# Optimization experiments

Measured on AMD Instinct MI355X. Metric: run time of the kernel, lower is better.

## Reference

```python
import math
import jax, jax.numpy as jnp
import numpy as np

NA = 50000   # number of query nodes
NB = 50000   # number of key/value nodes
E = 800000   # number of edges
CA = 256
CB = 256
D = 256
H = 8
DH = D // H


def setup_inputs() -> dict:
    key = jax.random.key(0)
    ks = jax.random.split(key, 8)
    s = 1.0 / math.sqrt(CA)
    return {
        "Fa": jax.random.normal(ks[0], (NA, CA), dtype=jnp.float32),
        "Fb": jax.random.normal(ks[1], (NB, CB), dtype=jnp.float32),
        "a_idx": jax.random.randint(ks[2], (E,), 0, NA, dtype=jnp.int64)
        if jax.config.jax_enable_x64 else jax.random.randint(ks[2], (E,), 0, NA, dtype=jnp.int32),
        "b_idx": jax.random.randint(ks[3], (E,), 0, NB, dtype=jnp.int64)
        if jax.config.jax_enable_x64 else jax.random.randint(ks[3], (E,), 0, NB, dtype=jnp.int32),
        # torch nn.Linear weights: (out_features, in_features), y = x @ W.T
        "Wq": jax.random.normal(ks[4], (D, CA), dtype=jnp.float32) * s,
        "Wk": jax.random.normal(ks[5], (D, CB), dtype=jnp.float32) * s,
        "Wv": jax.random.normal(ks[6], (D, CB), dtype=jnp.float32) * s,
        "Wproj": jax.random.normal(ks[7], (CA, D), dtype=jnp.float32) * s,
    }


def _edge_attention(Q, K, V, Q_idx, K_idx, n_queries):
    # Q: (Na,H,dh)  K,V: (Nb,H,dh)  Q_idx,K_idx: (E,)
    scale = 1.0 / math.sqrt(Q.shape[-1])
    logits = jnp.sum(Q[Q_idx] * K[K_idx], axis=-1) * scale      # (E, H)
    # segmented softmax over edges sharing the same query (per head)
    seg_max = jax.ops.segment_max(logits, Q_idx, num_segments=n_queries)  # (Na, H)
    seg_max = jnp.where(jnp.isfinite(seg_max), seg_max, 0.0)
    ex = jnp.exp(logits - seg_max[Q_idx])                        # (E, H)
    seg_sum = jax.ops.segment_sum(ex, Q_idx, num_segments=n_queries)      # (Na, H)
    weights = ex / jnp.maximum(seg_sum[Q_idx], 1e-30)            # (E, H)
    # scatter-add weighted values
    out = jax.ops.segment_sum(weights[..., None] * V[K_idx], Q_idx,
                              num_segments=n_queries)            # (Na, H, dh)
    return out


def reference(Fa, Fb, a_idx, b_idx, Wq, Wk, Wv, Wproj):
    Na = Fa.shape[0]
    Q = (Fa @ Wq.T).reshape(Na, H, DH)
    K = (Fb @ Wk.T).reshape(-1, H, DH)
    V = (Fb @ Wv.T).reshape(-1, H, DH)
    out = _edge_attention(Q, K, V, a_idx, b_idx, Na)
    out = out.reshape(Na, H * DH)
    return Fa + out @ Wproj.T
```

## Files before the change

kernel.cpp:

```cpp
#include <hip/hip_runtime.h>

#define DM 256

typedef __attribute__((ext_vector_type(8))) short bf16x8;
typedef __attribute__((ext_vector_type(4))) float f32x4;
typedef __attribute__((ext_vector_type(4))) unsigned short us16x4;
typedef unsigned short us16;

__device__ __forceinline__ unsigned short f2bf(float f) {
  unsigned int u = __float_as_uint(f);
  u += 0x7fffu + ((u >> 16) & 1u);
  return (unsigned short)(u >> 16);
}
__device__ __forceinline__ float bf2f(unsigned short s) {
  return __uint_as_float(((unsigned int)s) << 16);
}

__device__ __forceinline__ void gload16(const void* g, void* l) {
  __builtin_amdgcn_global_load_lds(
      (const __attribute__((address_space(1))) void*)g,
      (__attribute__((address_space(3))) void*)l, 16, 0, 0);
}

template <bool A_FP32>
__global__ __launch_bounds__(512) void gemm_bf16(
    const void* __restrict__ Avoid, const us16* __restrict__ W,
    us16* __restrict__ Cb, float* __restrict__ Cf, const float* __restrict__ R,
    int Mreal, int ldc)
{
  __shared__ us16 As[128 * 32];
  __shared__ us16 Bs[256 * 32];
  const int tid = threadIdx.x;
  const int w = tid >> 6, l = tid & 63;
  const int wr = w >> 2, wc = w & 3;
  const int rowBase = blockIdx.x * 128;
  const int colBase = blockIdx.y * 256;
  const int ar = tid >> 2, ac = (tid & 3) * 8;
  f32x4 acc[4][4] = {};

  for (int k0 = 0; k0 < 256; k0 += 32) {
#pragma unroll
    for (int j = 0; j < 2; ++j) {
      const int r0 = (w * 2 + j) * 16;
      gload16(W + (size_t)(colBase + r0 + (l >> 2)) * 256 + k0 + (l & 3) * 8,
              &Bs[r0 * 32]);
    }
    {
      const int grow = rowBase + ar;
      bf16x8 av = (bf16x8){0, 0, 0, 0, 0, 0, 0, 0};
      if (grow < Mreal) {
        if (A_FP32) {
          const float* Af = (const float*)Avoid;
          const float4 x = *(const float4*)(Af + (size_t)grow * 256 + k0 + ac);
          const float4 y = *(const float4*)(Af + (size_t)grow * 256 + k0 + ac + 4);
          av[0] = (short)f2bf(x.x); av[1] = (short)f2bf(x.y);
          av[2] = (short)f2bf(x.z); av[3] = (short)f2bf(x.w);
          av[4] = (short)f2bf(y.x); av[5] = (short)f2bf(y.y);
          av[6] = (short)f2bf(y.z); av[7] = (short)f2bf(y.w);
        } else {
          const us16* Ab = (const us16*)Avoid;
          av = *(const bf16x8*)(Ab + (size_t)grow * 256 + k0 + ac);
        }
      }
      *(bf16x8*)&As[ar * 32 + ac] = av;
    }
    __syncthreads();
    bf16x8 af[4], bfr[4];
#pragma unroll
    for (int m = 0; m < 4; ++m)
      af[m] = *(const bf16x8*)&As[(wr * 64 + m * 16 + (l & 15)) * 32 + (l >> 4) * 8];
#pragma unroll
    for (int n = 0; n < 4; ++n)
      bfr[n] = *(const bf16x8*)&Bs[(wc * 64 + n * 16 + (l & 15)) * 32 + (l >> 4) * 8];
#pragma unroll
    for (int m = 0; m < 4; ++m)
#pragma unroll
      for (int n = 0; n < 4; ++n)
        acc[m][n] = __builtin_amdgcn_mfma_f32_16x16x32_bf16(af[m], bfr[n], acc[m][n], 0, 0, 0);
    __syncthreads();
  }

  const int er = (l >> 4) * 4;
  const int ec = l & 15;
#pragma unroll
  for (int m = 0; m < 4; ++m)
#pragma unroll
    for (int n = 0; n < 4; ++n)
#pragma unroll
      for (int j = 0; j < 4; ++j) {
        const int grow = rowBase + wr * 64 + m * 16 + er + j;
        const int gcol = colBase + wc * 64 + n * 16 + ec;
        const float v = acc[m][n][j];
        if (Cf) {
          if (grow < Mreal) {
            const size_t off = (size_t)grow * ldc + gcol;
            Cf[off] = v + R[off];
          }
        } else {
          Cb[(size_t)grow * ldc + gcol] = f2bf(v);
        }
      }
}

__global__ void cvt_weights(const float* __restrict__ Wq, const float* __restrict__ Wk,
                            const float* __restrict__ Wv, const float* __restrict__ Wp,
                            us16* __restrict__ out)
{
  const int g = blockIdx.x * 256 + threadIdx.x;
  const size_t e = (size_t)g * 8;
  const int sel = (int)(e >> 16);
  const float* src = (sel == 0) ? Wq : (sel == 1) ? Wk : (sel == 2) ? Wv : Wp;
  const size_t loc = e & 65535;
  const float4 x = *(const float4*)(src + loc);
  const float4 y = *(const float4*)(src + loc + 4);
  bf16x8 o;
  o[0] = (short)f2bf(x.x); o[1] = (short)f2bf(x.y);
  o[2] = (short)f2bf(x.z); o[3] = (short)f2bf(x.w);
  o[4] = (short)f2bf(y.x); o[5] = (short)f2bf(y.y);
  o[6] = (short)f2bf(y.z); o[7] = (short)f2bf(y.w);
  *(bf16x8*)(out + e) = o;
}

__global__ void hist_kernel(const int* __restrict__ a_idx, int* __restrict__ counts, int E)
{
  const int e = blockIdx.x * 256 + threadIdx.x;
  if (e < E) atomicAdd(&counts[a_idx[e]], 1);
}

__global__ __launch_bounds__(256) void scan_offs(const int* __restrict__ counts,
    int* __restrict__ offs, int* __restrict__ cursor, int* __restrict__ total, int n)
{
  __shared__ int buf[256];
  __shared__ int sbase;
  const int t = threadIdx.x;
  const int i = blockIdx.x * 256 + t;
  const int v = (i < n) ? counts[i] : 0;
  buf[t] = v;
  __syncthreads();
#pragma unroll
  for (int off = 1; off < 256; off <<= 1) {
    const int x = (t >= off) ? buf[t - off] : 0;
    __syncthreads();
    buf[t] += x;
    __syncthreads();
  }
  const int incl = buf[t];
  if (t == 255) sbase = atomicAdd(total, incl);
  __syncthreads();
  if (i < n) {
    const int excl = sbase + incl - v;
    offs[i] = excl;
    cursor[i] = excl;
  }
}

__global__ void scatter_kernel(const int* __restrict__ a_idx, const int* __restrict__ b_idx,
    int* __restrict__ cursor, int* __restrict__ bel, int E)
{
  const int e = blockIdx.x * 256 + threadIdx.x;
  if (e < E) bel[atomicAdd(&cursor[a_idx[e]], 1)] = b_idx[e];
}

#define ATTN_STEP(K, V, J)                                     \
  if ((J) < cnt) {                                             \
    float p = q0 * bf2f(K[0]);                                 \
    p = fmaf(q1, bf2f(K[1]), p);                               \
    p = fmaf(q2, bf2f(K[2]), p);                               \
    p = fmaf(q3, bf2f(K[3]), p);                               \
    p += __shfl_xor(p, 1, 64);                                 \
    p += __shfl_xor(p, 2, 64);                                 \
    p += __shfl_xor(p, 4, 64);                                 \
    const float ex = __expf(p * scale);                        \
    ssum += ex;                                                \
    acc0 = fmaf(ex, bf2f(V[0]), acc0);                         \
    acc1 = fmaf(ex, bf2f(V[1]), acc1);                         \
    acc2 = fmaf(ex, bf2f(V[2]), acc2);                         \
    acc3 = fmaf(ex, bf2f(V[3]), acc3);                         \
  }

#define ATTN_LOAD(K, V, IDX)                                   \
  {                                                            \
    const us16* kv = KVb + (size_t)bel[start + (IDX)] * 512;   \
    K = *(const us16x4*)(kv + l * 4);                          \
    V = *(const us16x4*)(kv + 256 + l * 4);                    \
  }

__global__ __launch_bounds__(256) void edge_attn(
    const us16* __restrict__ Qb, const us16* __restrict__ KVb,
    const int* __restrict__ offs, const int* __restrict__ counts,
    const int* __restrict__ bel, us16* __restrict__ outb, int NA)
{
  const int a = blockIdx.x * 4 + (threadIdx.x >> 6);
  if (a >= NA) return;
  const int l = threadIdx.x & 63;
  const float scale = 0.17677669529663687f;

  const us16x4 q4 = *(const us16x4*)(Qb + (size_t)a * 256 + l * 4);
  const float q0 = bf2f(q4[0]), q1 = bf2f(q4[1]), q2 = bf2f(q4[2]), q3 = bf2f(q4[3]);

  const int start = offs[a];
  const int cnt = counts[a];
  float acc0 = 0.f, acc1 = 0.f, acc2 = 0.f, acc3 = 0.f, ssum = 0.f;

  if (cnt > 0) {
    const int last = cnt - 1;
    us16x4 ka, va, kb, vb, kc, vc, kd, vd;
    ATTN_LOAD(ka, va, 0)
    ATTN_LOAD(kb, vb, min(1, last))
    ATTN_LOAD(kc, vc, min(2, last))
    ATTN_LOAD(kd, vd, min(3, last))
    for (int i = 0; i < cnt; i += 4) {
      us16x4 na, xa, nb, xb, nc, xc, nd, xd;
      ATTN_LOAD(na, xa, min(i + 4, last))
      ATTN_LOAD(nb, xb, min(i + 5, last))
      ATTN_LOAD(nc, xc, min(i + 6, last))
      ATTN_LOAD(nd, xd, min(i + 7, last))
      ATTN_STEP(ka, va, i + 0)
      ATTN_STEP(kb, vb, i + 1)
      ATTN_STEP(kc, vc, i + 2)
      ATTN_STEP(kd, vd, i + 3)
      ka = na; va = xa; kb = nb; vb = xb;
      kc = nc; vc = xc; kd = nd; vd = xd;
    }
  }

  const float inv = (cnt > 0) ? 1.f / ssum : 0.f;
  us16x4 o;
  o[0] = f2bf(acc0 * inv); o[1] = f2bf(acc1 * inv);
  o[2] = f2bf(acc2 * inv); o[3] = f2bf(acc3 * inv);
  *(us16x4*)(outb + (size_t)a * 256 + l * 4) = o;
}

extern "C" void kernel_launch(void* const* d_in, const int* in_sizes, int n_in,
                              void* d_out, int out_size, void* d_ws, size_t ws_size,
                              hipStream_t stream)
{
  const float* Fa    = (const float*)d_in[0];
  const float* Fb    = (const float*)d_in[1];
  const int*   a_idx = (const int*)d_in[2];
  const int*   b_idx = (const int*)d_in[3];
  const float* Wq    = (const float*)d_in[4];
  const float* Wk    = (const float*)d_in[5];
  const float* Wv    = (const float*)d_in[6];
  const float* Wproj = (const float*)d_in[7];
  float* out = (float*)d_out;

  const int NA = in_sizes[0] / DM;
  const int NB = in_sizes[1] / DM;
  const int E  = in_sizes[2];
  const int MAp = (NA + 127) & ~127;
  const int NBp = (NB + 127) & ~127;

  us16* Qbf   = (us16*)d_ws;
  us16* KVbf  = Qbf   + (size_t)MAp * 256;
  us16* ATbf  = KVbf  + (size_t)NBp * 512;
  us16* W_all = ATbf  + (size_t)MAp * 256;
  int* total  = (int*)(W_all + 1024 * 256);
  int* counts = total + 1;
  int* offs   = counts + NA;
  int* cursor = offs + NA;
  int* bel    = cursor + NA;

  hipMemsetAsync(total, 0, (size_t)(NA + 1) * sizeof(int), stream);

  cvt_weights<<<128, 256, 0, stream>>>(Wq, Wk, Wv, Wproj, W_all);

  hist_kernel<<<(E + 255) / 256, 256, 0, stream>>>(a_idx, counts, E);
  scan_offs<<<(NA + 255) / 256, 256, 0, stream>>>(counts, offs, cursor, total, NA);
  scatter_kernel<<<(E + 255) / 256, 256, 0, stream>>>(a_idx, b_idx, cursor, bel, E);

  gemm_bf16<true><<<dim3(MAp / 128, 1), 512, 0, stream>>>(Fa, W_all, Qbf, nullptr, nullptr, NA, 256);
  gemm_bf16<true><<<dim3(NBp / 128, 2), 512, 0, stream>>>(Fb, W_all + 256 * 256, KVbf, nullptr, nullptr, NB, 512);

  edge_attn<<<(NA + 3) / 4, 256, 0, stream>>>(Qbf, KVbf, offs, counts, bel, ATbf, NA);

  gemm_bf16<false><<<dim3(MAp / 128, 1), 512, 0, stream>>>(ATbf, W_all + 768 * 256, nullptr, out, Fa, NA, 256);
}
```

Measured before the change: 437.9 us.

## Interleave K and V per lane and merge Q/K/V GEMM launches

The K/V GEMM epilogue now writes K and V interleaved in groups of four per lane, so the edge attention kernel fetches each neighbor's K and V with one 16-byte load per lane instead of two 8-byte loads. The Q and KV projections are combined into a single launch with a z-dimension selecting Q, K or V, removing one kernel launch and letting the three GEMMs share the GPU. The projection GEMM is split into its own specialized kernel. The interleaved epilogue stores are scattered within each row, which may make the GEMM writes less coalesced.

```diff
diff --git a/kernel.cpp b/kernel.cpp
--- a/kernel.cpp
+++ b/kernel.cpp
@@ -5,6 +5,7 @@
 typedef __attribute__((ext_vector_type(8))) short bf16x8;
 typedef __attribute__((ext_vector_type(4))) float f32x4;
 typedef __attribute__((ext_vector_type(4))) unsigned short us16x4;
+typedef __attribute__((ext_vector_type(8))) unsigned short us16x8;
 typedef unsigned short us16;
 
 __device__ __forceinline__ unsigned short f2bf(float f) {
@@ -22,19 +23,26 @@
       (__attribute__((address_space(3))) void*)l, 16, 0, 0);
 }
 
-template <bool A_FP32>
-__global__ __launch_bounds__(512) void gemm_bf16(
-    const void* __restrict__ Avoid, const us16* __restrict__ W,
-    us16* __restrict__ Cb, float* __restrict__ Cf, const float* __restrict__ R,
-    int Mreal, int ldc)
-{
+__global__ __launch_bounds__(512) void qkv_gemm(
+    const float* __restrict__ Fa, const float* __restrict__ Fb,
+    const us16* __restrict__ W_all, us16* __restrict__ Qbf,
+    us16* __restrict__ KVbf, int NA, int NB)
+{
+  const int z = blockIdx.z;
+  const float* A = (z == 0) ? Fa : Fb;
+  const int Mreal = (z == 0) ? NA : NB;
+  const int Mp = (Mreal + 127) & ~127;
+  const us16* W = W_all + (size_t)z * 256 * 256;
+  us16* Cb = (z == 0) ? Qbf : KVbf;
+  const int ldc = (z == 0) ? 256 : 512;
+
   __shared__ us16 As[128 * 32];
   __shared__ us16 Bs[256 * 32];
   const int tid = threadIdx.x;
   const int w = tid >> 6, l = tid & 63;
   const int wr = w >> 2, wc = w & 3;
   const int rowBase = blockIdx.x * 128;
-  const int colBase = blockIdx.y * 256;
+  if (rowBase >= Mp) return;
   const int ar = tid >> 2, ac = (tid & 3) * 8;
   f32x4 acc[4][4] = {};
 
@@ -42,25 +50,18 @@
 #pragma unroll
     for (int j = 0; j < 2; ++j) {
       const int r0 = (w * 2 + j) * 16;
-      gload16(W + (size_t)(colBase + r0 + (l >> 2)) * 256 + k0 + (l & 3) * 8,
-              &Bs[r0 * 32]);
+      gload16(W + (size_t)(r0 + (l >> 2)) * 256 + k0 + (l & 3) * 8, &Bs[r0 * 32]);
     }
     {
       const int grow = rowBase + ar;
       bf16x8 av = (bf16x8){0, 0, 0, 0, 0, 0, 0, 0};
       if (grow < Mreal) {
-        if (A_FP32) {
-          const float* Af = (const float*)Avoid;
-          const float4 x = *(const float4*)(Af + (size_t)grow * 256 + k0 + ac);
-          const float4 y = *(const float4*)(Af + (size_t)grow * 256 + k0 + ac + 4);
-          av[0] = (short)f2bf(x.x); av[1] = (short)f2bf(x.y);
-          av[2] = (short)f2bf(x.z); av[3] = (short)f2bf(x.w);
-          av[4] = (short)f2bf(y.x); av[5] = (short)f2bf(y.y);
-          av[6] = (short)f2bf(y.z); av[7] = (short)f2bf(y.w);
-        } else {
-          const us16* Ab = (const us16*)Avoid;
-          av = *(const bf16x8*)(Ab + (size_t)grow * 256 + k0 + ac);
-        }
+        const float4 x = *(const float4*)(A + (size_t)grow * 256 + k0 + ac);
+        const float4 y = *(const float4*)(A + (size_t)grow * 256 + k0 + ac + 4);
+        av[0] = (short)f2bf(x.x); av[1] = (short)f2bf(x.y);
+        av[2] = (short)f2bf(x.z); av[3] = (short)f2bf(x.w);
+        av[4] = (short)f2bf(y.x); av[5] = (short)f2bf(y.y);
+        av[6] = (short)f2bf(y.z); av[7] = (short)f2bf(y.w);
       }
       *(bf16x8*)&As[ar * 32 + ac] = av;
     }
@@ -82,6 +83,7 @@
 
   const int er = (l >> 4) * 4;
   const int ec = l & 15;
+  const int vofs = (z == 2) ? 4 : 0;
 #pragma unroll
   for (int m = 0; m < 4; ++m)
 #pragma unroll
@@ -89,15 +91,61 @@
 #pragma unroll
       for (int j = 0; j < 4; ++j) {
         const int grow = rowBase + wr * 64 + m * 16 + er + j;
-        const int gcol = colBase + wc * 64 + n * 16 + ec;
-        const float v = acc[m][n][j];
-        if (Cf) {
-          if (grow < Mreal) {
-            const size_t off = (size_t)grow * ldc + gcol;
-            Cf[off] = v + R[off];
-          }
-        } else {
-          Cb[(size_t)grow * ldc + gcol] = f2bf(v);
+        const int c = wc * 64 + n * 16 + ec;
+        const int col = (z == 0) ? c : ((c >> 2) * 8 + (c & 3) + vofs);
+        Cb[(size_t)grow * ldc + col] = f2bf(acc[m][n][j]);
+      }
+}
+
+__global__ __launch_bounds__(512) void proj_gemm(
+    const us16* __restrict__ A, const us16* __restrict__ W,
+    float* __restrict__ Cf, const float* __restrict__ R, int Mreal)
+{
+  __shared__ us16 As[128 * 32];
+  __shared__ us16 Bs[256 * 32];
+  const int tid = threadIdx.x;
+  const int w = tid >> 6, l = tid & 63;
+  const int wr = w >> 2, wc = w & 3;
+  const int rowBase = blockIdx.x * 128;
+  const int ar = tid >> 2, ac = (tid & 3) * 8;
+  f32x4 acc[4][4] = {};
+
+  for (int k0 = 0; k0 < 256; k0 += 32) {
+#pragma unroll
+    for (int j = 0; j < 2; ++j) {
+      const int r0 = (w * 2 + j) * 16;
+      gload16(W + (size_t)(r0 + (l >> 2)) * 256 + k0 + (l & 3) * 8, &Bs[r0 * 32]);
+    }
+    *(bf16x8*)&As[ar * 32 + ac] =
+        *(const bf16x8*)(A + (size_t)(rowBase + ar) * 256 + k0 + ac);
+    __syncthreads();
+    bf16x8 af[4], bfr[4];
+#pragma unroll
+    for (int m = 0; m < 4; ++m)
+      af[m] = *(const bf16x8*)&As[(wr * 64 + m * 16 + (l & 15)) * 32 + (l >> 4) * 8];
+#pragma unroll
+    for (int n = 0; n < 4; ++n)
+      bfr[n] = *(const bf16x8*)&Bs[(wc * 64 + n * 16 + (l & 15)) * 32 + (l >> 4) * 8];
+#pragma unroll
+    for (int m = 0; m < 4; ++m)
+#pragma unroll
+      for (int n = 0; n < 4; ++n)
+        acc[m][n] = __builtin_amdgcn_mfma_f32_16x16x32_bf16(af[m], bfr[n], acc[m][n], 0, 0, 0);
+    __syncthreads();
+  }
+
+  const int er = (l >> 4) * 4;
+  const int ec = l & 15;
+#pragma unroll
+  for (int m = 0; m < 4; ++m)
+#pragma unroll
+    for (int n = 0; n < 4; ++n)
+#pragma unroll
+      for (int j = 0; j < 4; ++j) {
+        const int grow = rowBase + wr * 64 + m * 16 + er + j;
+        if (grow < Mreal) {
+          const size_t off = (size_t)grow * 256 + wc * 64 + n * 16 + ec;
+          Cf[off] = acc[m][n][j] + R[off];
         }
       }
 }
@@ -161,29 +209,25 @@
   if (e < E) bel[atomicAdd(&cursor[a_idx[e]], 1)] = b_idx[e];
 }
 
-#define ATTN_STEP(K, V, J)                                     \
+#define ATTN_STEP(S, J)                                        \
   if ((J) < cnt) {                                             \
-    float p = q0 * bf2f(K[0]);                                 \
-    p = fmaf(q1, bf2f(K[1]), p);                               \
-    p = fmaf(q2, bf2f(K[2]), p);                               \
-    p = fmaf(q3, bf2f(K[3]), p);                               \
+    float p = q0 * bf2f(S[0]);                                 \
+    p = fmaf(q1, bf2f(S[1]), p);                               \
+    p = fmaf(q2, bf2f(S[2]), p);                               \
+    p = fmaf(q3, bf2f(S[3]), p);                               \
     p += __shfl_xor(p, 1, 64);                                 \
     p += __shfl_xor(p, 2, 64);                                 \
     p += __shfl_xor(p, 4, 64);                                 \
     const float ex = __expf(p * scale);                        \
     ssum += ex;                                                \
-    acc0 = fmaf(ex, bf2f(V[0]), acc0);                         \
-    acc1 = fmaf(ex, bf2f(V[1]), acc1);                         \
-    acc2 = fmaf(ex, bf2f(V[2]), acc2);                         \
-    acc3 = fmaf(ex, bf2f(V[3]), acc3);                         \
-  }
-
-#define ATTN_LOAD(K, V, IDX)                                   \
-  {                                                            \
-    const us16* kv = KVb + (size_t)bel[start + (IDX)] * 512;   \
-    K = *(const us16x4*)(kv + l * 4);                          \
-    V = *(const us16x4*)(kv + 256 + l * 4);                    \
-  }
+    acc0 = fmaf(ex, bf2f(S[4]), acc0);                         \
+    acc1 = fmaf(ex, bf2f(S[5]), acc1);                         \
+    acc2 = fmaf(ex, bf2f(S[6]), acc2);                         \
+    acc3 = fmaf(ex, bf2f(S[7]), acc3);                         \
+  }
+
+#define ATTN_LOAD(S, IDX)                                      \
+  S = *(const us16x8*)(KVb + (size_t)bel[start + (IDX)] * 512 + l * 8);
 
 __global__ __launch_bounds__(256) void edge_attn(
     const us16* __restrict__ Qb, const us16* __restrict__ KVb,
@@ -204,23 +248,22 @@
 
   if (cnt > 0) {
     const int last = cnt - 1;
-    us16x4 ka, va, kb, vb, kc, vc, kd, vd;
-    ATTN_LOAD(ka, va, 0)
-    ATTN_LOAD(kb, vb, min(1, last))
-    ATTN_LOAD(kc, vc, min(2, last))
-    ATTN_LOAD(kd, vd, min(3, last))
+    us16x8 sa, sb, sc, sd;
+    ATTN_LOAD(sa, 0)
+    ATTN_LOAD(sb, min(1, last))
+    ATTN_LOAD(sc, min(2, last))
+    ATTN_LOAD(sd, min(3, last))
     for (int i = 0; i < cnt; i += 4) {
-      us16x4 na, xa, nb, xb, nc, xc, nd, xd;
-      ATTN_LOAD(na, xa, min(i + 4, last))
-      ATTN_LOAD(nb, xb, min(i + 5, last))
-      ATTN_LOAD(nc, xc, min(i + 6, last))
-      ATTN_LOAD(nd, xd, min(i + 7, last))
-      ATTN_STEP(ka, va, i + 0)
-      ATTN_STEP(kb, vb, i + 1)
-      ATTN_STEP(kc, vc, i + 2)
-      ATTN_STEP(kd, vd, i + 3)
-      ka = na; va = xa; kb = nb; vb = xb;
-      kc = nc; vc = xc; kd = nd; vd = xd;
+      us16x8 na, nb, nc, nd;
+      ATTN_LOAD(na, min(i + 4, last))
+      ATTN_LOAD(nb, min(i + 5, last))
+      ATTN_LOAD(nc, min(i + 6, last))
+      ATTN_LOAD(nd, min(i + 7, last))
+      ATTN_STEP(sa, i + 0)
+      ATTN_STEP(sb, i + 1)
+      ATTN_STEP(sc, i + 2)
+      ATTN_STEP(sd, i + 3)
+      sa = na; sb = nb; sc = nc; sd = nd;
     }
   }
 
@@ -250,6 +293,7 @@
   const int E  = in_sizes[2];
   const int MAp = (NA + 127) & ~127;
   const int NBp = (NB + 127) & ~127;
+  const int MXp = (MAp > NBp) ? MAp : NBp;
 
   us16* Qbf   = (us16*)d_ws;
   us16* KVbf  = Qbf   + (size_t)MAp * 256;
@@ -269,10 +313,9 @@
   scan_offs<<<(NA + 255) / 256, 256, 0, stream>>>(counts, offs, cursor, total, NA);
   scatter_kernel<<<(E + 255) / 256, 256, 0, stream>>>(a_idx, b_idx, cursor, bel, E);
 
-  gemm_bf16<true><<<dim3(MAp / 128, 1), 512, 0, stream>>>(Fa, W_all, Qbf, nullptr, nullptr, NA, 256);
-  gemm_bf16<true><<<dim3(NBp / 128, 2), 512, 0, stream>>>(Fb, W_all + 256 * 256, KVbf, nullptr, nullptr, NB, 512);
+  qkv_gemm<<<dim3(MXp / 128, 1, 3), 512, 0, stream>>>(Fa, Fb, W_all, Qbf, KVbf, NA, NB);
 
   edge_attn<<<(NA + 3) / 4, 256, 0, stream>>>(Qbf, KVbf, offs, counts, bel, ATbf, NA);
 
-  gemm_bf16<false><<<dim3(MAp / 128, 1), 512, 0, stream>>>(ATbf, W_all + 768 * 256, nullptr, out, Fa, NA, 256);
-}
+  proj_gemm<<<dim3(MAp / 128, 1), 512, 0, stream>>>(ATbf, W_all + 768 * 256, out, Fa, NA);
+}
```

New measurement: 448.3 us. +2.4%, slower.
